# Optimization experiments

Hardware: AMD Instinct MI355X
Metric: run time of the kernel (lower is better)

The kernel has to match this reference:

```python
import jax, jax.numpy as jnp
import numpy as np

HEADS = 16
D_K = 64  # hidden_size // heads = 1024 // 16
SCALE = D_K ** 0.5


def setup_inputs() -> dict:
    key = jax.random.key(0)
    ks = jax.random.split(key, 7)
    B, S, D = 4, 2048, 1024
    H = 1024  # hidden_size
    O = 1024  # outputs_dims
    s = 0.02
    return {
        "query": jax.random.normal(ks[0], (B, S, D), dtype=jnp.float32),
        "key": jax.random.normal(ks[1], (B, S, D), dtype=jnp.float32),
        "value": jax.random.normal(ks[2], (B, S, D), dtype=jnp.float32),
        "Wq": jax.random.normal(ks[3], (D, H), dtype=jnp.float32) * s,
        "Wk": jax.random.normal(ks[4], (D, H), dtype=jnp.float32) * s,
        "Wv": jax.random.normal(ks[5], (D, H), dtype=jnp.float32) * s,
        "Wo": jax.random.normal(ks[6], (H, O), dtype=jnp.float32) * s,
    }


def reference(query, key, value, Wq, Wk, Wv, Wo):
    B, S, _ = query.shape
    # Dense projections with relu activation (as in the original module)
    q = jax.nn.relu(query @ Wq).reshape(B, S, HEADS, D_K)  # [B,S,H,dk]
    k = jax.nn.relu(key @ Wk).reshape(B, S, HEADS, D_K)
    v = jax.nn.relu(value @ Wv).reshape(B, S, HEADS, D_K)
    # scores: [B,H,Sq,Sk]
    scores = jnp.einsum('bqhd,bkhd->bhqk', q, k) / SCALE
    attn = jax.nn.softmax(scores, axis=-1)
    # attention-weighted values -> [B,Sq,H,dk] -> [B,Sq,H*dk]
    ctx = jnp.einsum('bhqk,bkhd->bqhd', attn, v).reshape(B, S, HEADS * D_K)
    out = jax.nn.relu(ctx @ Wo)
    return out
```

## Files before the change

### kernel.cpp

```cpp
#include <hip/hip_runtime.h>

typedef unsigned short u16;
typedef __bf16 bf16x8 __attribute__((ext_vector_type(8)));
typedef float f32x4 __attribute__((ext_vector_type(4)));
typedef u16 u16x8 __attribute__((ext_vector_type(8)));
typedef u16 u16x4 __attribute__((ext_vector_type(4)));

#define MFMA16(a, b, c) __builtin_amdgcn_mfma_f32_16x16x32_bf16(a, b, c, 0, 0, 0)

static constexpr float QSC = 0.18033688011112042f;

__device__ inline u16 f2bf(float f) {
  union { float f; unsigned u; } x; x.f = f;
  unsigned r = x.u + 0x7FFF + ((x.u >> 16) & 1);
  return (u16)(r >> 16);
}
__device__ inline u16 cvt_bf(float f) {
  __bf16 h = (__bf16)f; return __builtin_bit_cast(u16, h);
}
__device__ inline bf16x8 ld_frag(const u16* p) {
  return __builtin_bit_cast(bf16x8, *(const u16x8*)p);
}
__device__ inline void dma16(const u16* g, u16* l) {
  __builtin_amdgcn_global_load_lds(
      (const __attribute__((address_space(1))) unsigned*)g,
      (__attribute__((address_space(3))) unsigned*)l, 16, 0, 0);
}

#if __has_builtin(__builtin_amdgcn_exp2f)
#define EXP2(x) __builtin_amdgcn_exp2f(x)
#else
#define EXP2(x) exp2f(x)
#endif

__launch_bounds__(256)
__global__ void prep_w(const float* __restrict__ Wq, const float* __restrict__ Wk,
                       const float* __restrict__ Wv, const float* __restrict__ Wo,
                       u16* __restrict__ Wt) {
  __shared__ u16 T[64 * 72];
  const int z = blockIdx.z;
  const float* W = z == 0 ? Wq : z == 1 ? Wk : z == 2 ? Wv : Wo;
  u16* D = Wt + ((size_t)z << 20);
  const int k0 = blockIdx.y * 64, c0 = blockIdx.x * 64;
  const int tid = threadIdx.x;
  const int kr = tid >> 2, cs = (tid & 3) * 16;
  const float* src = W + (size_t)(k0 + kr) * 1024 + c0 + cs;
  float f[16];
#pragma unroll
  for (int i = 0; i < 4; ++i) *(float4*)&f[i * 4] = ((const float4*)src)[i];
#pragma unroll
  for (int i = 0; i < 16; ++i) T[(cs + i) * 72 + kr] = cvt_bf(f[i]);
  __syncthreads();
  const int nn = tid >> 2, ks = (tid & 3) * 16;
  u16* dst = D + (size_t)(c0 + nn) * 1024 + k0 + ks;
  *(u16x8*)dst = *(u16x8*)&T[nn * 72 + ks];
  *(u16x8*)(dst + 8) = *(u16x8*)&T[nn * 72 + ks + 8];
}

__launch_bounds__(256)
__global__ void prep_a(const float* __restrict__ q, const float* __restrict__ k,
                       const float* __restrict__ v, u16* __restrict__ dq,
                       u16* __restrict__ dk, u16* __restrict__ dv) {
  const int z = blockIdx.z;
  const float* s = z == 0 ? q : z == 1 ? k : v;
  u16* d = z == 0 ? dq : z == 1 ? dk : dv;
  for (size_t i = blockIdx.x * 256 + threadIdx.x; i < (size_t)1048576; i += 262144) {
    const float* g = s + i * 8;
    float4 f0 = *(const float4*)g, f1 = *(const float4*)(g + 4);
    u16x8 h;
    h[0] = cvt_bf(f0.x); h[1] = cvt_bf(f0.y); h[2] = cvt_bf(f0.z); h[3] = cvt_bf(f0.w);
    h[4] = cvt_bf(f1.x); h[5] = cvt_bf(f1.y); h[6] = cvt_bf(f1.z); h[7] = cvt_bf(f1.w);
    *(u16x8*)(d + i * 8) = h;
  }
}

__launch_bounds__(256, 2)
__global__ void gemm_fwd(const u16* __restrict__ Aq, const u16* __restrict__ Ak,
                         const u16* __restrict__ Av, const u16* __restrict__ Wt,
                         u16* __restrict__ Qw, u16* __restrict__ Kw,
                         u16* __restrict__ Vw) {
  __shared__ u16 smem[32768];
  const int z = blockIdx.z;
  const u16* A = z == 0 ? Aq : z == 1 ? Ak : Av;
  const u16* Bt = Wt + ((size_t)z << 20);
  u16* out = z == 0 ? Qw : z == 1 ? Kw : Vw;
  const u16* Aop = (z == 2) ? Bt : A;
  const u16* Bop = (z == 2) ? A : Bt;

  const int tid = threadIdx.x;
  const int lane = tid & 63, l15 = lane & 15, quad = lane >> 4;
  const int wv = tid >> 6, wm = wv & 1, wn = wv >> 1;
  int m0, n0;
  if (z == 2) {
    const int id = blockIdx.y * 32 + blockIdx.x;
    m0 = (id >> 6) * 256;
    n0 = (id & 63) * 128;
  } else {
    const int mblk = ((blockIdx.x & 7) << 2) | (blockIdx.x >> 3);
    m0 = mblk * 256;
    n0 = blockIdx.y * 128;
  }

  const u16* gA[4];
#pragma unroll
  for (int i = 0; i < 4; ++i) gA[i] = Aop + (size_t)(m0 + tid) * 1024 + i * 8;
  const u16* gB[2];
#pragma unroll
  for (int i = 0; i < 2; ++i)
    gB[i] = Bop + (size_t)(n0 + (tid & 127)) * 1024 + (i * 2 + (tid >> 7)) * 8;

  const int offA = (quad * 256 + wm * 128 + l15) * 8;
  const int offB = 8192 + (quad * 128 + wn * 64 + l15) * 8;

  f32x4 acc[8][4] = {};

#pragma unroll
  for (int i = 0; i < 4; ++i) dma16(gA[i], &smem[i * 2048 + wv * 512]);
#pragma unroll
  for (int i = 0; i < 2; ++i) dma16(gB[i], &smem[8192 + i * 2048 + wv * 512]);
  asm volatile("s_waitcnt vmcnt(0)" ::: "memory");
  __builtin_amdgcn_sched_barrier(0);
  __builtin_amdgcn_s_barrier();

#pragma unroll 1
  for (int t = 0; t < 32; ++t) {
    const int bo = (t & 1) ? 12288 : 0;
    const int nbo = (t & 1) ? 0 : 12288;
    if (t + 1 < 32) {
#pragma unroll
      for (int i = 0; i < 4; ++i)
        dma16(gA[i] + (t + 1) * 32, &smem[nbo + i * 2048 + wv * 512]);
    }
    bf16x8 a[4], b[4];
#pragma unroll
    for (int j = 0; j < 4; ++j) b[j] = ld_frag(&smem[bo + offB + j * 128]);
#pragma unroll
    for (int i = 0; i < 4; ++i) a[i] = ld_frag(&smem[bo + offA + i * 128]);
    asm volatile("s_waitcnt lgkmcnt(0)" ::: "memory");
    __builtin_amdgcn_sched_barrier(0);
    __builtin_amdgcn_s_setprio(1);
#pragma unroll
    for (int i = 0; i < 4; ++i)
#pragma unroll
      for (int j = 0; j < 4; ++j)
        acc[i][j] = MFMA16(a[i], b[j], acc[i][j]);
    __builtin_amdgcn_s_setprio(0);
    __builtin_amdgcn_s_barrier();
    if (t + 1 < 32) {
#pragma unroll
      for (int i = 0; i < 2; ++i)
        dma16(gB[i] + (t + 1) * 32, &smem[nbo + 8192 + i * 2048 + wv * 512]);
    }
#pragma unroll
    for (int i = 0; i < 4; ++i) a[i] = ld_frag(&smem[bo + offA + (4 + i) * 128]);
    asm volatile("s_waitcnt lgkmcnt(0)" ::: "memory");
    __builtin_amdgcn_sched_barrier(0);
    __builtin_amdgcn_s_setprio(1);
#pragma unroll
    for (int i = 0; i < 4; ++i)
#pragma unroll
      for (int j = 0; j < 4; ++j)
        acc[4 + i][j] = MFMA16(a[i], b[j], acc[4 + i][j]);
    __builtin_amdgcn_s_setprio(0);
    if (t + 1 < 32) {
      asm volatile("s_waitcnt vmcnt(0)" ::: "memory");
      __builtin_amdgcn_sched_barrier(0);
    }
    __builtin_amdgcn_s_barrier();
  }

  if (z < 2) {
    const float sc = z == 0 ? QSC : 1.0f;
#pragma unroll
    for (int i = 0; i < 8; ++i)
#pragma unroll
      for (int j = 0; j < 4; ++j)
#pragma unroll
        for (int r = 0; r < 4; ++r) {
          float v = fmaxf(acc[i][j][r], 0.f) * sc;
          int m = m0 + wm * 128 + i * 16 + quad * 4 + r;
          int n = n0 + wn * 64 + j * 16 + l15;
          out[(size_t)m * 1024 + n] = f2bf(v);
        }
  } else {
    const int bb = n0 >> 11, s0 = n0 & 2047;
    __syncthreads();
#pragma unroll
    for (int i = 0; i < 8; ++i)
#pragma unroll
      for (int j = 0; j < 4; ++j)
#pragma unroll
        for (int r = 0; r < 4; ++r) {
          const int row = wm * 128 + i * 16 + quad * 4 + r;
          const int col = wn * 64 + j * 16 + l15;
          smem[row * 128 + col] = f2bf(fmaxf(acc[i][j][r], 0.f));
        }
    __syncthreads();
#pragma unroll
    for (int i2 = 0; i2 < 16; ++i2) {
      const int c = i2 * 256 + tid;
      const int row = c >> 4, ch = c & 15;
      u16* dst = out + (size_t)(bb * 1024 + m0 + row) * 2048 + s0 + ch * 8;
      *(u16x8*)dst = *(u16x8*)&smem[row * 128 + ch * 8];
    }
  }
}

__launch_bounds__(256, 2)
__global__ void gemm_out(const u16* __restrict__ A, const u16* __restrict__ Bt,
                         float* __restrict__ out) {
  __shared__ u16 smem[24576];
  const int tid = threadIdx.x;
  const int lane = tid & 63, l15 = lane & 15, quad = lane >> 4;
  const int wv = tid >> 6, wm = wv & 1, wn = wv >> 1;
  const int mblk = ((blockIdx.x & 7) << 2) | (blockIdx.x >> 3);
  const int m0 = mblk * 256;
  const int n0 = blockIdx.y * 128;

  const u16* gA[4];
#pragma unroll
  for (int i = 0; i < 4; ++i) gA[i] = A + (size_t)(m0 + tid) * 1024 + i * 8;
  const u16* gB[2];
#pragma unroll
  for (int i = 0; i < 2; ++i)
    gB[i] = Bt + (size_t)(n0 + (tid & 127)) * 1024 + (i * 2 + (tid >> 7)) * 8;

  const int offA = (quad * 256 + wm * 128 + l15) * 8;
  const int offB = 8192 + (quad * 128 + wn * 64 + l15) * 8;

  f32x4 acc[8][4] = {};

#pragma unroll
  for (int i = 0; i < 4; ++i) dma16(gA[i], &smem[i * 2048 + wv * 512]);
#pragma unroll
  for (int i = 0; i < 2; ++i) dma16(gB[i], &smem[8192 + i * 2048 + wv * 512]);
  asm volatile("s_waitcnt vmcnt(0)" ::: "memory");
  __builtin_amdgcn_sched_barrier(0);
  __builtin_amdgcn_s_barrier();

#pragma unroll 1
  for (int t = 0; t < 32; ++t) {
    const int bo = (t & 1) ? 12288 : 0;
    const int nbo = (t & 1) ? 0 : 12288;
    if (t + 1 < 32) {
#pragma unroll
      for (int i = 0; i < 4; ++i)
        dma16(gA[i] + (t + 1) * 32, &smem[nbo + i * 2048 + wv * 512]);
    }
    bf16x8 a[4], b[4];
#pragma unroll
    for (int j = 0; j < 4; ++j) b[j] = ld_frag(&smem[bo + offB + j * 128]);
#pragma unroll
    for (int i = 0; i < 4; ++i) a[i] = ld_frag(&smem[bo + offA + i * 128]);
    asm volatile("s_waitcnt lgkmcnt(0)" ::: "memory");
    __builtin_amdgcn_sched_barrier(0);
    __builtin_amdgcn_s_setprio(1);
#pragma unroll
    for (int i = 0; i < 4; ++i)
#pragma unroll
      for (int j = 0; j < 4; ++j)
        acc[i][j] = MFMA16(a[i], b[j], acc[i][j]);
    __builtin_amdgcn_s_setprio(0);
    __builtin_amdgcn_s_barrier();
    if (t + 1 < 32) {
#pragma unroll
      for (int i = 0; i < 2; ++i)
        dma16(gB[i] + (t + 1) * 32, &smem[nbo + 8192 + i * 2048 + wv * 512]);
    }
#pragma unroll
    for (int i = 0; i < 4; ++i) a[i] = ld_frag(&smem[bo + offA + (4 + i) * 128]);
    asm volatile("s_waitcnt lgkmcnt(0)" ::: "memory");
    __builtin_amdgcn_sched_barrier(0);
    __builtin_amdgcn_s_setprio(1);
#pragma unroll
    for (int i = 0; i < 4; ++i)
#pragma unroll
      for (int j = 0; j < 4; ++j)
        acc[4 + i][j] = MFMA16(a[i], b[j], acc[4 + i][j]);
    __builtin_amdgcn_s_setprio(0);
    if (t + 1 < 32) {
      asm volatile("s_waitcnt vmcnt(0)" ::: "memory");
      __builtin_amdgcn_sched_barrier(0);
    }
    __builtin_amdgcn_s_barrier();
  }

#pragma unroll
  for (int i = 0; i < 8; ++i)
#pragma unroll
    for (int j = 0; j < 4; ++j)
#pragma unroll
      for (int r = 0; r < 4; ++r) {
        int m = m0 + wm * 128 + i * 16 + quad * 4 + r;
        int n = n0 + wn * 64 + j * 16 + l15;
        out[(size_t)m * 1024 + n] = fmaxf(acc[i][j][r], 0.f);
      }
}

__launch_bounds__(256, 2)
__global__ void attn(const u16* __restrict__ Q, const u16* __restrict__ K,
                     const u16* __restrict__ V, u16* __restrict__ ctx) {
  __shared__ u16 Ksm[2][4096];
  __shared__ u16 Vsm[2][4096];
  __shared__ u16 Psm[4][4096];

  const int tid = threadIdx.x;
  const int lane = tid & 63, l15 = lane & 15, quad = lane >> 4;
  const int wv = tid >> 6;
  const int bh = blockIdx.x, b = bh >> 4, h = bh & 15;
  const int q0 = blockIdx.y * 256 + wv * 64;

  const u16* Kb = K + ((size_t)b * 2048) * 1024 + h * 64;
  const u16* Vb = V + (size_t)bh * 64 * 2048;
  u16* Pw = Psm[wv];

  const int ck0 = tid, ck1 = 256 + tid;
  const u16* kg0 = Kb + (size_t)(ck0 & 63) * 1024 + (ck0 >> 6) * 8;
  const u16* kg1 = Kb + (size_t)(ck1 & 63) * 1024 + (ck1 >> 6) * 8;
  const u16* vg0 = Vb + (size_t)(ck0 & 63) * 2048 + (ck0 >> 6) * 8;
  const u16* vg1 = Vb + (size_t)(ck1 & 63) * 2048 + (ck1 >> 6) * 8;

  bf16x8 aq[4][2];
#pragma unroll
  for (int qh = 0; qh < 4; ++qh)
#pragma unroll
    for (int kk = 0; kk < 2; ++kk)
      aq[qh][kk] = ld_frag(Q + (size_t)(b * 2048 + q0 + qh * 16 + l15) * 1024 +
                           h * 64 + kk * 32 + quad * 8);

  f32x4 o[4][4] = {};
  float ls[4] = {0.f, 0.f, 0.f, 0.f};

  dma16(kg0, &Ksm[0][ck0 * 8]);
  dma16(kg1, &Ksm[0][ck1 * 8]);
  dma16(vg0, &Vsm[0][ck0 * 8]);
  dma16(vg1, &Vsm[0][ck1 * 8]);

#pragma unroll 1
  for (int t = 0; t < 32; ++t) {
    const int cur = t & 1, nxt = cur ^ 1;
    __syncthreads();

    if (t + 1 < 32) {
      const int kadv = (t + 1) * 64;
      dma16(kg0 + (size_t)kadv * 1024, &Ksm[nxt][ck0 * 8]);
      dma16(kg1 + (size_t)kadv * 1024, &Ksm[nxt][ck1 * 8]);
      dma16(vg0 + kadv, &Vsm[nxt][ck0 * 8]);
      dma16(vg1 + kadv, &Vsm[nxt][ck1 * 8]);
    }

    bf16x8 kf[2][4];
#pragma unroll
    for (int kk = 0; kk < 2; ++kk)
#pragma unroll
      for (int jj = 0; jj < 4; ++jj)
        kf[kk][jj] = ld_frag(&Ksm[cur][((kk * 4 + quad) * 64 + jj * 16 + l15) * 8]);

    f32x4 st[4][4] = {};
    asm volatile("s_waitcnt lgkmcnt(0)" ::: "memory");
    __builtin_amdgcn_sched_barrier(0);
    __builtin_amdgcn_s_setprio(1);
#pragma unroll
    for (int kk = 0; kk < 2; ++kk)
#pragma unroll
      for (int jj = 0; jj < 4; ++jj)
#pragma unroll
        for (int qh = 0; qh < 4; ++qh)
          st[qh][jj] = MFMA16(kf[kk][jj], aq[qh][kk], st[qh][jj]);
    __builtin_amdgcn_s_setprio(0);

#pragma unroll
    for (int qh = 0; qh < 4; ++qh)
#pragma unroll
      for (int jj = 0; jj < 4; ++jj) {
        float p0 = EXP2(st[qh][jj][0]), p1 = EXP2(st[qh][jj][1]);
        float p2 = EXP2(st[qh][jj][2]), p3 = EXP2(st[qh][jj][3]);
        ls[qh] += (p0 + p1) + (p2 + p3);
        u16x4 pk;
        pk[0] = cvt_bf(p0); pk[1] = cvt_bf(p1);
        pk[2] = cvt_bf(p2); pk[3] = cvt_bf(p3);
        const int kc = jj * 2 + (quad >> 1);
        *(u16x4*)&Pw[(kc * 64 + qh * 16 + l15) * 8 + (quad & 1) * 4] = pk;
      }

#pragma unroll
    for (int kk = 0; kk < 2; ++kk) {
      bf16x8 pa[4];
#pragma unroll
      for (int qh = 0; qh < 4; ++qh)
        pa[qh] = ld_frag(&Pw[((kk * 4 + quad) * 64 + qh * 16 + l15) * 8]);
      asm volatile("s_waitcnt lgkmcnt(0)" ::: "memory");
      __builtin_amdgcn_sched_barrier(0);
      __builtin_amdgcn_s_setprio(1);
#pragma unroll
      for (int j = 0; j < 4; ++j) {
        bf16x8 vb = ld_frag(&Vsm[cur][((kk * 4 + quad) * 64 + j * 16 + l15) * 8]);
#pragma unroll
        for (int qh = 0; qh < 4; ++qh)
          o[qh][j] = MFMA16(vb, pa[qh], o[qh][j]);
      }
      __builtin_amdgcn_s_setprio(0);
    }
  }

  float inv[4];
#pragma unroll
  for (int qh = 0; qh < 4; ++qh) {
    ls[qh] += __shfl_xor(ls[qh], 16, 64);
    ls[qh] += __shfl_xor(ls[qh], 32, 64);
    inv[qh] = 1.f / ls[qh];
  }

#pragma unroll
  for (int qh = 0; qh < 4; ++qh) {
    const int tok = b * 2048 + q0 + qh * 16 + l15;
#pragma unroll
    for (int j = 0; j < 4; ++j) {
      u16x4 pk;
#pragma unroll
      for (int r = 0; r < 4; ++r) pk[r] = cvt_bf(o[qh][j][r] * inv[qh]);
      *(u16x4*)&ctx[(size_t)tok * 1024 + h * 64 + j * 16 + quad * 4] = pk;
    }
  }
}

extern "C" void kernel_launch(void* const* d_in, const int* in_sizes, int n_in,
                              void* d_out, int out_size, void* d_ws, size_t ws_size,
                              hipStream_t stream) {
  const float* query = (const float*)d_in[0];
  const float* key   = (const float*)d_in[1];
  const float* value = (const float*)d_in[2];
  const float* Wq = (const float*)d_in[3];
  const float* Wk = (const float*)d_in[4];
  const float* Wv = (const float*)d_in[5];
  const float* Wo = (const float*)d_in[6];
  float* outp = (float*)d_out;

  u16* Wt  = (u16*)d_ws;
  u16* Awq = Wt + ((size_t)4 << 20);
  u16* Qw  = Awq + ((size_t)8 << 20);
  u16* Kw  = Qw + ((size_t)8 << 20);
  u16* Vt  = Kw + ((size_t)8 << 20);
  u16* Awk = (u16*)d_out;
  u16* Awv = Awk + ((size_t)8 << 20);
  u16* Cw  = Awq;

  prep_w<<<dim3(16, 16, 4), 256, 0, stream>>>(Wq, Wk, Wv, Wo, Wt);
  prep_a<<<dim3(1024, 1, 3), 256, 0, stream>>>(query, key, value, Awq, Awk, Awv);
  gemm_fwd<<<dim3(32, 8, 3), 256, 0, stream>>>(Awq, Awk, Awv, Wt, Qw, Kw, Vt);
  attn<<<dim3(64, 8), 256, 0, stream>>>(Qw, Kw, Vt, Cw);
  gemm_out<<<dim3(32, 8), 256, 0, stream>>>(Cw, Wt + ((size_t)3 << 20), outp);
}
```

Before: 368.0 us.

## Enlarge GEMM tiles to 256x256 with 512 threads and K-step 64

The projection GEMM now uses 512-thread blocks computing 256x256 output tiles, and both GEMMs use a K step of 64 with 16 iterations instead of 32. This halves the number of barrier-separated main-loop iterations and raises data reuse per loaded tile. It also drops the mid-iteration barrier. The V-transpose epilogue is split into two halves so it fits the shared buffer. In exchange, shared memory per block doubles (128KB for gemm_fwd), which may limit blocks per CU, and the projection grid shrinks to 384 blocks.

```diff
diff --git a/kernel.cpp b/kernel.cpp
--- a/kernel.cpp
+++ b/kernel.cpp
@@ -74,12 +74,12 @@
   }
 }
 
-__launch_bounds__(256, 2)
+__launch_bounds__(512, 2)
 __global__ void gemm_fwd(const u16* __restrict__ Aq, const u16* __restrict__ Ak,
                          const u16* __restrict__ Av, const u16* __restrict__ Wt,
                          u16* __restrict__ Qw, u16* __restrict__ Kw,
                          u16* __restrict__ Vw) {
-  __shared__ u16 smem[32768];
+  __shared__ u16 smem[65536];
   const int z = blockIdx.z;
   const u16* A = z == 0 ? Aq : z == 1 ? Ak : Av;
   const u16* Bt = Wt + ((size_t)z << 20);
@@ -90,48 +90,42 @@
   const int tid = threadIdx.x;
   const int lane = tid & 63, l15 = lane & 15, quad = lane >> 4;
   const int wv = tid >> 6, wm = wv & 1, wn = wv >> 1;
-  int m0, n0;
-  if (z == 2) {
-    const int id = blockIdx.y * 32 + blockIdx.x;
-    m0 = (id >> 6) * 256;
-    n0 = (id & 63) * 128;
-  } else {
-    const int mblk = ((blockIdx.x & 7) << 2) | (blockIdx.x >> 3);
-    m0 = mblk * 256;
-    n0 = blockIdx.y * 128;
-  }
+  const int mblk = ((blockIdx.x & 7) << 2) | (blockIdx.x >> 3);
+  const int m0 = (z == 2) ? blockIdx.y * 256 : mblk * 256;
+  const int n0 = (z == 2) ? mblk * 256 : blockIdx.y * 256;
 
   const u16* gA[4];
-#pragma unroll
-  for (int i = 0; i < 4; ++i) gA[i] = Aop + (size_t)(m0 + tid) * 1024 + i * 8;
-  const u16* gB[2];
-#pragma unroll
-  for (int i = 0; i < 2; ++i)
-    gB[i] = Bop + (size_t)(n0 + (tid & 127)) * 1024 + (i * 2 + (tid >> 7)) * 8;
+  const u16* gB[4];
+#pragma unroll
+  for (int i = 0; i < 4; ++i) {
+    const int c = i * 512 + tid;
+    gA[i] = Aop + (size_t)(m0 + (c & 255)) * 1024 + (c >> 8) * 8;
+    gB[i] = Bop + (size_t)(n0 + (c & 255)) * 1024 + (c >> 8) * 8;
+  }
 
   const int offA = (quad * 256 + wm * 128 + l15) * 8;
-  const int offB = 8192 + (quad * 128 + wn * 64 + l15) * 8;
+  const int offB = 16384 + (quad * 256 + wn * 64 + l15) * 8;
 
   f32x4 acc[8][4] = {};
 
 #pragma unroll
-  for (int i = 0; i < 4; ++i) dma16(gA[i], &smem[i * 2048 + wv * 512]);
-#pragma unroll
-  for (int i = 0; i < 2; ++i) dma16(gB[i], &smem[8192 + i * 2048 + wv * 512]);
+  for (int i = 0; i < 4; ++i) dma16(gA[i], &smem[i * 4096 + wv * 512]);
+#pragma unroll
+  for (int i = 0; i < 4; ++i) dma16(gB[i], &smem[16384 + i * 4096 + wv * 512]);
   asm volatile("s_waitcnt vmcnt(0)" ::: "memory");
   __builtin_amdgcn_sched_barrier(0);
   __builtin_amdgcn_s_barrier();
 
 #pragma unroll 1
-  for (int t = 0; t < 32; ++t) {
-    const int bo = (t & 1) ? 12288 : 0;
-    const int nbo = (t & 1) ? 0 : 12288;
-    if (t + 1 < 32) {
+  for (int t = 0; t < 16; ++t) {
+    const int bo = (t & 1) ? 32768 : 0;
+    const int nbo = bo ^ 32768;
+    bf16x8 a[4], b[4];
+    if (t < 15) {
 #pragma unroll
       for (int i = 0; i < 4; ++i)
-        dma16(gA[i] + (t + 1) * 32, &smem[nbo + i * 2048 + wv * 512]);
-    }
-    bf16x8 a[4], b[4];
+        dma16(gA[i] + (t + 1) * 64, &smem[nbo + i * 4096 + wv * 512]);
+    }
 #pragma unroll
     for (int j = 0; j < 4; ++j) b[j] = ld_frag(&smem[bo + offB + j * 128]);
 #pragma unroll
@@ -145,14 +139,9 @@
       for (int j = 0; j < 4; ++j)
         acc[i][j] = MFMA16(a[i], b[j], acc[i][j]);
     __builtin_amdgcn_s_setprio(0);
-    __builtin_amdgcn_s_barrier();
-    if (t + 1 < 32) {
-#pragma unroll
-      for (int i = 0; i < 2; ++i)
-        dma16(gB[i] + (t + 1) * 32, &smem[nbo + 8192 + i * 2048 + wv * 512]);
-    }
-#pragma unroll
-    for (int i = 0; i < 4; ++i) a[i] = ld_frag(&smem[bo + offA + (4 + i) * 128]);
+#pragma unroll
+    for (int i = 0; i < 4; ++i)
+      a[i] = ld_frag(&smem[bo + offA + (4 + i) * 128]);
     asm volatile("s_waitcnt lgkmcnt(0)" ::: "memory");
     __builtin_amdgcn_sched_barrier(0);
     __builtin_amdgcn_s_setprio(1);
@@ -162,7 +151,39 @@
       for (int j = 0; j < 4; ++j)
         acc[4 + i][j] = MFMA16(a[i], b[j], acc[4 + i][j]);
     __builtin_amdgcn_s_setprio(0);
-    if (t + 1 < 32) {
+    if (t < 15) {
+#pragma unroll
+      for (int i = 0; i < 4; ++i)
+        dma16(gB[i] + (t + 1) * 64, &smem[nbo + 16384 + i * 4096 + wv * 512]);
+    }
+#pragma unroll
+    for (int j = 0; j < 4; ++j)
+      b[j] = ld_frag(&smem[bo + offB + 8192 + j * 128]);
+#pragma unroll
+    for (int i = 0; i < 4; ++i)
+      a[i] = ld_frag(&smem[bo + offA + 8192 + i * 128]);
+    asm volatile("s_waitcnt lgkmcnt(0)" ::: "memory");
+    __builtin_amdgcn_sched_barrier(0);
+    __builtin_amdgcn_s_setprio(1);
+#pragma unroll
+    for (int i = 0; i < 4; ++i)
+#pragma unroll
+      for (int j = 0; j < 4; ++j)
+        acc[i][j] = MFMA16(a[i], b[j], acc[i][j]);
+    __builtin_amdgcn_s_setprio(0);
+#pragma unroll
+    for (int i = 0; i < 4; ++i)
+      a[i] = ld_frag(&smem[bo + offA + 8192 + (4 + i) * 128]);
+    asm volatile("s_waitcnt lgkmcnt(0)" ::: "memory");
+    __builtin_amdgcn_sched_barrier(0);
+    __builtin_amdgcn_s_setprio(1);
+#pragma unroll
+    for (int i = 0; i < 4; ++i)
+#pragma unroll
+      for (int j = 0; j < 4; ++j)
+        acc[4 + i][j] = MFMA16(a[i], b[j], acc[4 + i][j]);
+    __builtin_amdgcn_s_setprio(0);
+    if (t < 15) {
       asm volatile("s_waitcnt vmcnt(0)" ::: "memory");
       __builtin_amdgcn_sched_barrier(0);
     }
@@ -184,24 +205,30 @@
         }
   } else {
     const int bb = n0 >> 11, s0 = n0 & 2047;
-    __syncthreads();
-#pragma unroll
-    for (int i = 0; i < 8; ++i)
-#pragma unroll
-      for (int j = 0; j < 4; ++j)
-#pragma unroll
-        for (int r = 0; r < 4; ++r) {
-          const int row = wm * 128 + i * 16 + quad * 4 + r;
-          const int col = wn * 64 + j * 16 + l15;
-          smem[row * 128 + col] = f2bf(fmaxf(acc[i][j][r], 0.f));
-        }
-    __syncthreads();
-#pragma unroll
-    for (int i2 = 0; i2 < 16; ++i2) {
-      const int c = i2 * 256 + tid;
-      const int row = c >> 4, ch = c & 15;
-      u16* dst = out + (size_t)(bb * 1024 + m0 + row) * 2048 + s0 + ch * 8;
-      *(u16x8*)dst = *(u16x8*)&smem[row * 128 + ch * 8];
+#pragma unroll
+    for (int half = 0; half < 2; ++half) {
+      __syncthreads();
+      if ((wn >> 1) == half) {
+#pragma unroll
+        for (int i = 0; i < 8; ++i)
+#pragma unroll
+          for (int j = 0; j < 4; ++j)
+#pragma unroll
+            for (int r = 0; r < 4; ++r) {
+              const int row = wm * 128 + i * 16 + quad * 4 + r;
+              const int col = (wn & 1) * 64 + j * 16 + l15;
+              smem[row * 128 + col] = f2bf(fmaxf(acc[i][j][r], 0.f));
+            }
+      }
+      __syncthreads();
+#pragma unroll
+      for (int i2 = 0; i2 < 8; ++i2) {
+        const int c = i2 * 512 + tid;
+        const int row = c >> 4, ch = c & 15;
+        u16* dst = out + (size_t)(bb * 1024 + m0 + row) * 2048 + s0 +
+                   half * 128 + ch * 8;
+        *(u16x8*)dst = *(u16x8*)&smem[row * 128 + ch * 8];
+      }
     }
   }
 }
@@ -209,7 +236,7 @@
 __launch_bounds__(256, 2)
 __global__ void gemm_out(const u16* __restrict__ A, const u16* __restrict__ Bt,
                          float* __restrict__ out) {
-  __shared__ u16 smem[24576];
+  __shared__ u16 smem[49152];
   const int tid = threadIdx.x;
   const int lane = tid & 63, l15 = lane & 15, quad = lane >> 4;
   const int wv = tid >> 6, wm = wv & 1, wn = wv >> 1;
@@ -217,41 +244,78 @@
   const int m0 = mblk * 256;
   const int n0 = blockIdx.y * 128;
 
-  const u16* gA[4];
-#pragma unroll
-  for (int i = 0; i < 4; ++i) gA[i] = A + (size_t)(m0 + tid) * 1024 + i * 8;
-  const u16* gB[2];
-#pragma unroll
-  for (int i = 0; i < 2; ++i)
-    gB[i] = Bt + (size_t)(n0 + (tid & 127)) * 1024 + (i * 2 + (tid >> 7)) * 8;
+  const u16* gA[8];
+#pragma unroll
+  for (int i = 0; i < 8; ++i) {
+    const int c = i * 256 + tid;
+    gA[i] = A + (size_t)(m0 + (c & 255)) * 1024 + (c >> 8) * 8;
+  }
+  const u16* gB[4];
+#pragma unroll
+  for (int i = 0; i < 4; ++i) {
+    const int c = i * 256 + tid;
+    gB[i] = Bt + (size_t)(n0 + (c & 127)) * 1024 + (c >> 7) * 8;
+  }
 
   const int offA = (quad * 256 + wm * 128 + l15) * 8;
-  const int offB = 8192 + (quad * 128 + wn * 64 + l15) * 8;
+  const int offB = 16384 + (quad * 128 + wn * 64 + l15) * 8;
 
   f32x4 acc[8][4] = {};
 
 #pragma unroll
-  for (int i = 0; i < 4; ++i) dma16(gA[i], &smem[i * 2048 + wv * 512]);
-#pragma unroll
-  for (int i = 0; i < 2; ++i) dma16(gB[i], &smem[8192 + i * 2048 + wv * 512]);
+  for (int i = 0; i < 8; ++i) dma16(gA[i], &smem[i * 2048 + wv * 512]);
+#pragma unroll
+  for (int i = 0; i < 4; ++i) dma16(gB[i], &smem[16384 + i * 2048 + wv * 512]);
   asm volatile("s_waitcnt vmcnt(0)" ::: "memory");
   __builtin_amdgcn_sched_barrier(0);
   __builtin_amdgcn_s_barrier();
 
 #pragma unroll 1
-  for (int t = 0; t < 32; ++t) {
-    const int bo = (t & 1) ? 12288 : 0;
-    const int nbo = (t & 1) ? 0 : 12288;
-    if (t + 1 < 32) {
+  for (int t = 0; t < 16; ++t) {
+    const int bo = (t & 1) ? 24576 : 0;
+    const int nbo = bo ^ 24576;
+    bf16x8 a[4], b[4];
+    if (t < 15) {
+#pragma unroll
+      for (int i = 0; i < 8; ++i)
+        dma16(gA[i] + (t + 1) * 64, &smem[nbo + i * 2048 + wv * 512]);
+    }
+#pragma unroll
+    for (int j = 0; j < 4; ++j) b[j] = ld_frag(&smem[bo + offB + j * 128]);
+#pragma unroll
+    for (int i = 0; i < 4; ++i) a[i] = ld_frag(&smem[bo + offA + i * 128]);
+    asm volatile("s_waitcnt lgkmcnt(0)" ::: "memory");
+    __builtin_amdgcn_sched_barrier(0);
+    __builtin_amdgcn_s_setprio(1);
+#pragma unroll
+    for (int i = 0; i < 4; ++i)
+#pragma unroll
+      for (int j = 0; j < 4; ++j)
+        acc[i][j] = MFMA16(a[i], b[j], acc[i][j]);
+    __builtin_amdgcn_s_setprio(0);
+#pragma unroll
+    for (int i = 0; i < 4; ++i)
+      a[i] = ld_frag(&smem[bo + offA + (4 + i) * 128]);
+    asm volatile("s_waitcnt lgkmcnt(0)" ::: "memory");
+    __builtin_amdgcn_sched_barrier(0);
+    __builtin_amdgcn_s_setprio(1);
+#pragma unroll
+    for (int i = 0; i < 4; ++i)
+#pragma unroll
+      for (int j = 0; j < 4; ++j)
+        acc[4 + i][j] = MFMA16(a[i], b[j], acc[4 + i][j]);
+    __builtin_amdgcn_s_setprio(0);
+    if (t < 15) {
 #pragma unroll
       for (int i = 0; i < 4; ++i)
-        dma16(gA[i] + (t + 1) * 32, &smem[nbo + i * 2048 + wv * 512]);
-    }
-    bf16x8 a[4], b[4];
-#pragma unroll
-    for (int j = 0; j < 4; ++j) b[j] = ld_frag(&smem[bo + offB + j * 128]);
-#pragma unroll
-    for (int i = 0; i < 4; ++i) a[i] = ld_frag(&smem[bo + offA + i * 128]);
+        dma16(gB[i] + (t + 1) * 64, &smem[nbo + 16384 + i * 2048 + wv * 512]);
+    }
+#pragma unroll
+    for (int j = 0; j < 4; ++j)
+      b[j] = ld_frag(&smem[bo + offB + 4096 + j * 128]);
+#pragma unroll
+    for (int i = 0; i < 4; ++i)
+      a[i] = ld_frag(&smem[bo + offA + 8192 + i * 128]);
     asm volatile("s_waitcnt lgkmcnt(0)" ::: "memory");
     __builtin_amdgcn_sched_barrier(0);
     __builtin_amdgcn_s_setprio(1);
@@ -261,14 +325,9 @@
       for (int j = 0; j < 4; ++j)
         acc[i][j] = MFMA16(a[i], b[j], acc[i][j]);
     __builtin_amdgcn_s_setprio(0);
-    __builtin_amdgcn_s_barrier();
-    if (t + 1 < 32) {
-#pragma unroll
-      for (int i = 0; i < 2; ++i)
-        dma16(gB[i] + (t + 1) * 32, &smem[nbo + 8192 + i * 2048 + wv * 512]);
-    }
-#pragma unroll
-    for (int i = 0; i < 4; ++i) a[i] = ld_frag(&smem[bo + offA + (4 + i) * 128]);
+#pragma unroll
+    for (int i = 0; i < 4; ++i)
+      a[i] = ld_frag(&smem[bo + offA + 8192 + (4 + i) * 128]);
     asm volatile("s_waitcnt lgkmcnt(0)" ::: "memory");
     __builtin_amdgcn_sched_barrier(0);
     __builtin_amdgcn_s_setprio(1);
@@ -278,7 +337,7 @@
       for (int j = 0; j < 4; ++j)
         acc[4 + i][j] = MFMA16(a[i], b[j], acc[4 + i][j]);
     __builtin_amdgcn_s_setprio(0);
-    if (t + 1 < 32) {
+    if (t < 15) {
       asm volatile("s_waitcnt vmcnt(0)" ::: "memory");
       __builtin_amdgcn_sched_barrier(0);
     }
@@ -447,7 +506,7 @@
 
   prep_w<<<dim3(16, 16, 4), 256, 0, stream>>>(Wq, Wk, Wv, Wo, Wt);
   prep_a<<<dim3(1024, 1, 3), 256, 0, stream>>>(query, key, value, Awq, Awk, Awv);
-  gemm_fwd<<<dim3(32, 8, 3), 256, 0, stream>>>(Awq, Awk, Awv, Wt, Qw, Kw, Vt);
+  gemm_fwd<<<dim3(32, 4, 3), 512, 0, stream>>>(Awq, Awk, Awv, Wt, Qw, Kw, Vt);
   attn<<<dim3(64, 8), 256, 0, stream>>>(Qw, Kw, Vt, Cw);
   gemm_out<<<dim3(32, 8), 256, 0, stream>>>(Cw, Wt + ((size_t)3 << 20), outp);
 }
```

After: 364.7 us. Within noise of the previous version (-0.9%).
